# Kernel optimization log

Measured on AMD Instinct MI355X. Metric: run time of the kernel, lower is better.

## Reference

```python
import jax, jax.numpy as jnp
import numpy as np

B, S, D = 8, 1024, 1024
NEG = -1e9


def setup_inputs() -> dict:
    key = jax.random.key(0)
    ks = jax.random.split(key, 6)
    context = jax.random.normal(ks[0], (B, S, D), dtype=jnp.float32)
    eos_mask = jax.random.randint(ks[1], (B, S, S), 0, 2).astype(jnp.int32)
    scale = 1.0 / np.sqrt(D).astype(np.float32)
    Wq = jax.random.normal(ks[2], (D, D), dtype=jnp.float32) * scale
    bq = jnp.zeros((D,), jnp.float32)
    Wk = jax.random.normal(ks[3], (D, D), dtype=jnp.float32) * scale
    bk = jnp.zeros((D,), jnp.float32)
    ln_a = jnp.ones((D,), jnp.float32)
    ln_b = jnp.zeros((D,), jnp.float32)
    return dict(context=context, eos_mask=eos_mask, Wq=Wq, bq=bq, Wk=Wk, bk=bk,
                ln_a=ln_a, ln_b=ln_b)


def _forward(context, eos_mask, Wq, bq, Wk, bk, ln_a, ln_b):
    d_model = context.shape[-1]
    seq_len = context.shape[1]
    # LayerNorm with torch-style unbiased std (ddof=1)
    mean = context.mean(-1, keepdims=True)
    var = ((context - mean) ** 2).sum(-1, keepdims=True) / (d_model - 1)
    x = ln_a * (context - mean) / (jnp.sqrt(var) + 1e-6) + ln_b

    a = jnp.eye(seq_len, k=1, dtype=jnp.int32)    # super-diagonal
    b = jnp.eye(seq_len, k=0, dtype=jnp.int32)    # diagonal
    c = jnp.eye(seq_len, k=-1, dtype=jnp.int32)   # sub-diagonal
    tri = jnp.triu(jnp.ones((seq_len, seq_len), jnp.float32), 0)

    mask = eos_mask & (a + c)  # [B,S,S] banded + eos mask

    q = x @ Wq.T + bq
    k = x @ Wk.T + bk
    scores = jnp.einsum('bsd,btd->bst', q, k) / d_model
    scores = jnp.where(mask == 0, NEG, scores)
    neibor = jax.nn.softmax(scores, axis=-1)
    neibor = jnp.sqrt(neibor * jnp.swapaxes(neibor, -2, -1) + 1e-9)

    # log-space triangular matmul 'scan'
    t = jnp.where(a == 0, 0.0, jnp.log(neibor + 1e-9)) @ tri  # [B,S,S]
    g = jnp.exp(jnp.einsum('st,btu->bsu', tri, t))
    strict_upper = tri.astype(jnp.int32) - b
    g = jnp.where(strict_upper == 0, 0.0, g)
    g = g + jnp.swapaxes(g, -2, -1) + jnp.where(b == 0, 1e-9, neibor)
    return g, neibor


def reference(context, eos_mask, Wq, bq, Wk, bk, ln_a, ln_b):
    return _forward(context, eos_mask, Wq, bq, Wk, bk, ln_a, ln_b)
```

## Files before the change

### kernel.cpp

```cpp
#include <hip/hip_runtime.h>
#include <math.h>

#define B_ 8
#define S_ 1024
#define D_ 1024
constexpr int BS = B_ * S_;

typedef short bf16x8 __attribute__((ext_vector_type(8)));
typedef float f32x4 __attribute__((ext_vector_type(4)));

__device__ __forceinline__ unsigned short f2bf(float f) {
    unsigned int u = __float_as_uint(f);
    u += 0x7fffu + ((u >> 16) & 1u);
    return (unsigned short)(u >> 16);
}
__device__ __forceinline__ float bf2f(unsigned short h) {
    return __uint_as_float(((unsigned int)h) << 16);
}

__device__ __forceinline__ float block_reduce_sum(float val, float* sh) {
    int tid = threadIdx.x;
    int lane = tid & 63, w = tid >> 6;
    #pragma unroll
    for (int off = 32; off > 0; off >>= 1) val += __shfl_down(val, off, 64);
    if (lane == 0) sh[w] = val;
    __syncthreads();
    int nw = blockDim.x >> 6;
    float total = 0.f;
    for (int i = 0; i < nw; i++) total += sh[i];
    __syncthreads();
    return total;
}

__device__ __forceinline__ float wave_reduce_sum(float v) {
    #pragma unroll
    for (int off = 32; off > 0; off >>= 1) v += __shfl_xor(v, off, 64);
    return v;
}

__global__ __launch_bounds__(256) void ln_kernel(
    const float* __restrict__ ctx,
    const float* __restrict__ ln_a,
    const float* __restrict__ ln_b,
    const float* __restrict__ u,
    const float* __restrict__ v,
    unsigned short* __restrict__ xb,
    float* __restrict__ au, float* __restrict__ av) {
    int wid = threadIdx.x >> 6, lane = threadIdx.x & 63;
    int r = blockIdx.x * 4 + wid;
    const float* row = ctx + (size_t)r * D_;
    float4 x[4];
    #pragma unroll
    for (int j = 0; j < 4; j++)
        x[j] = *(const float4*)(row + lane * 4 + j * 256);
    float s = 0.f;
    #pragma unroll
    for (int j = 0; j < 4; j++) s += x[j].x + x[j].y + x[j].z + x[j].w;
    s = wave_reduce_sum(s);
    float mean = s * (1.0f / D_);
    float sq = 0.f;
    #pragma unroll
    for (int j = 0; j < 4; j++) {
        float dx = x[j].x - mean, dy = x[j].y - mean;
        float dz = x[j].z - mean, dw = x[j].w - mean;
        sq += dx * dx + dy * dy + dz * dz + dw * dw;
    }
    sq = wave_reduce_sum(sq);
    float var = sq * (1.0f / (D_ - 1));
    float inv = 1.0f / (sqrtf(var) + 1e-6f);
    float pu = 0.f, pv = 0.f;
    #pragma unroll
    for (int j = 0; j < 4; j++) {
        int d0 = lane * 4 + j * 256;
        float4 a4 = *(const float4*)(ln_a + d0);
        float4 b4 = *(const float4*)(ln_b + d0);
        float y0 = a4.x * (x[j].x - mean) * inv + b4.x;
        float y1 = a4.y * (x[j].y - mean) * inv + b4.y;
        float y2 = a4.z * (x[j].z - mean) * inv + b4.z;
        float y3 = a4.w * (x[j].w - mean) * inv + b4.w;
        ushort4 o;
        o.x = f2bf(y0); o.y = f2bf(y1); o.z = f2bf(y2); o.w = f2bf(y3);
        *(ushort4*)(xb + (size_t)r * D_ + d0) = o;
        float4 u4 = *(const float4*)(u + d0);
        float4 v4 = *(const float4*)(v + d0);
        pu += u4.x * y0 + u4.y * y1 + u4.z * y2 + u4.w * y3;
        pv += v4.x * y0 + v4.y * y1 + v4.z * y2 + v4.w * y3;
    }
    pu = wave_reduce_sum(pu);
    pv = wave_reduce_sum(pv);
    if (lane == 0) { au[r] = pu; av[r] = pv; }
}

__global__ void prep_kernel(const float* __restrict__ Wq, const float* __restrict__ Wk,
                            const float* __restrict__ bq, const float* __restrict__ bk,
                            unsigned short* __restrict__ Wqt,
                            unsigned short* __restrict__ Wkt,
                            float* __restrict__ u, float* __restrict__ v,
                            float* __restrict__ c0) {
    int bid = blockIdx.x;
    int tid = threadIdx.x;
    if (bid < 2048) {
        __shared__ float t[32][33];
        const float* in = (bid < 1024) ? Wq : Wk;
        unsigned short* out = (bid < 1024) ? Wqt : Wkt;
        int bb = bid & 1023;
        int bx = (bb & 31) * 32, by = (bb >> 5) * 32;
        int tx = tid & 31, ty = tid >> 5;
        #pragma unroll
        for (int i = 0; i < 32; i += 8)
            t[ty + i][tx] = in[(size_t)(by + ty + i) * D_ + bx + tx];
        __syncthreads();
        #pragma unroll
        for (int i = 0; i < 32; i += 8)
            out[(size_t)(bx + ty + i) * D_ + by + tx] = f2bf(t[tx][ty + i]);
    } else {
        int b = bid - 2048;
        if (b == 128) {
            __shared__ float sh2[4];
            float p = 0.f;
            #pragma unroll
            for (int i = 0; i < 4; i++) {
                int d = tid + i * 256;
                p += bq[d] * bk[d];
            }
            float tot = block_reduce_sum(p, sh2);
            if (tid == 0) atomicAdd(c0, tot);
        } else {
            float ua[4] = {}, va[4] = {};
            int d0 = b * 8;
            for (int d = d0; d < d0 + 8; d++) {
                float bqd = bq[d], bkd = bk[d];
                const float* wkr = Wk + (size_t)d * D_;
                const float* wqr = Wq + (size_t)d * D_;
                #pragma unroll
                for (int i = 0; i < 4; i++) {
                    int c = tid + i * 256;
                    ua[i] += wkr[c] * bqd;
                    va[i] += wqr[c] * bkd;
                }
            }
            #pragma unroll
            for (int i = 0; i < 4; i++) {
                atomicAdd(&u[tid + i * 256], ua[i]);
                atomicAdd(&v[tid + i * 256], va[i]);
            }
        }
    }
}

__global__ __launch_bounds__(256) void gemm_bt64(
    const unsigned short* __restrict__ A,
    const unsigned short* __restrict__ Bt,
    unsigned short* __restrict__ C,
    int M, int N, int K) {
    __shared__ __align__(16) unsigned short smem[16384];
    const int tid = threadIdx.x;
    const int wave = tid >> 6, lane = tid & 63;
    const int bm = blockIdx.y * 64, bn = blockIdx.x * 64;
    const int lrow8 = lane >> 3;
    const int pchunk = lane & 7;
    const int m_lane = lane & 15, quad = lane >> 4;
    const int wr = wave >> 1, wc = wave & 1;

    f32x4 acc[2][2] = {};

    auto stage = [&](int buf, int k0) {
        unsigned short* As = smem + buf * 8192;
        unsigned short* Bs = As + 4096;
        #pragma unroll
        for (int c = 0; c < 2; c++) {
            int row = wave * 16 + c * 8 + lrow8;
            int gchunk = pchunk ^ (row & 7);
            const unsigned short* gpA = A + (size_t)(bm + row) * K + k0 + gchunk * 8;
            const unsigned short* gpB = Bt + (size_t)(bn + row) * K + k0 + gchunk * 8;
            __builtin_amdgcn_global_load_lds(
                (const __attribute__((address_space(1))) void*)gpA,
                (__attribute__((address_space(3))) void*)(As + (wave * 16 + c * 8) * 64),
                16, 0, 0);
            __builtin_amdgcn_global_load_lds(
                (const __attribute__((address_space(1))) void*)gpB,
                (__attribute__((address_space(3))) void*)(Bs + (wave * 16 + c * 8) * 64),
                16, 0, 0);
        }
    };

    const int nt = K >> 6;
    stage(0, 0);
    __syncthreads();
    int cur = 0;
    for (int t = 0; t < nt; ++t) {
        if (t < nt - 1) stage(cur ^ 1, (t + 1) * 64);
        const unsigned short* As = smem + cur * 8192;
        const unsigned short* Bs = As + 4096;
        #pragma unroll
        for (int kk = 0; kk < 2; kk++) {
            bf16x8 af[2], bfr[2];
            #pragma unroll
            for (int i = 0; i < 2; i++) {
                int row = wr * 32 + i * 16 + m_lane;
                int lchunk = kk * 4 + quad;
                af[i] = *(const bf16x8*)(As + row * 64 + (lchunk ^ (row & 7)) * 8);
            }
            #pragma unroll
            for (int j = 0; j < 2; j++) {
                int row = wc * 32 + j * 16 + m_lane;
                int lchunk = kk * 4 + quad;
                bfr[j] = *(const bf16x8*)(Bs + row * 64 + (lchunk ^ (row & 7)) * 8);
            }
            #pragma unroll
            for (int i = 0; i < 2; i++)
                #pragma unroll
                for (int j = 0; j < 2; j++)
                    acc[i][j] = __builtin_amdgcn_mfma_f32_16x16x32_bf16(
                        af[i], bfr[j], acc[i][j], 0, 0, 0);
        }
        __syncthreads();
        cur ^= 1;
    }
    #pragma unroll
    for (int i = 0; i < 2; i++)
        #pragma unroll
        for (int j = 0; j < 2; j++)
            #pragma unroll
            for (int r = 0; r < 4; r++) {
                int row = bm + wr * 32 + i * 16 + quad * 4 + r;
                int col = bn + wc * 32 + j * 16 + m_lane;
                C[(size_t)row * N + col] = f2bf(acc[i][j][r]);
            }
}

__device__ __forceinline__ int xs_idx(int row, int col) {
    return row * 128 + (((col >> 3) ^ (row & 7)) << 3) + (col & 7);
}

__global__ __launch_bounds__(256) void gemm_fused(
    const unsigned short* __restrict__ A,
    const unsigned short* __restrict__ Bt,
    float* __restrict__ ydu, float* __restrict__ ydd,
    int M, int N, int K) {
    __shared__ __align__(16) unsigned short smem[32768];
    const int tid = threadIdx.x;
    const int wave = tid >> 6, lane = tid & 63;
    const int bid = blockIdx.x;
    const int bm = (bid & 63) * 128, bn = (bid >> 6) * 128;
    const int lrow8 = lane >> 3;
    const int pchunk = lane & 7;
    const int m_lane = lane & 15, quad = lane >> 4;
    const int wr = wave >> 1, wc = wave & 1;

    f32x4 acc[4][4] = {};

    auto stage = [&](int buf, int k0) {
        unsigned short* As = smem + buf * 16384;
        unsigned short* Bs = As + 8192;
        #pragma unroll
        for (int c = 0; c < 4; c++) {
            int row = wave * 32 + c * 8 + lrow8;
            int gchunk = pchunk ^ (row & 7);
            const unsigned short* gpA = A + (size_t)(bm + row) * K + k0 + gchunk * 8;
            __builtin_amdgcn_global_load_lds(
                (const __attribute__((address_space(1))) void*)gpA,
                (__attribute__((address_space(3))) void*)(As + (wave * 32 + c * 8) * 64),
                16, 0, 0);
            const unsigned short* gpB = Bt + (size_t)(bn + row) * K + k0 + gchunk * 8;
            __builtin_amdgcn_global_load_lds(
                (const __attribute__((address_space(1))) void*)gpB,
                (__attribute__((address_space(3))) void*)(Bs + (wave * 32 + c * 8) * 64),
                16, 0, 0);
        }
    };

    const int nt = K >> 6;
    stage(0, 0);
    __syncthreads();
    int cur = 0;
    for (int t = 0; t < nt; ++t) {
        if (t < nt - 1) stage(cur ^ 1, (t + 1) * 64);
        const unsigned short* As = smem + cur * 16384;
        const unsigned short* Bs = As + 8192;
        #pragma unroll
        for (int kk = 0; kk < 2; kk++) {
            bf16x8 af[4], bfr[4];
            #pragma unroll
            for (int i = 0; i < 4; i++) {
                int row = wr * 64 + i * 16 + m_lane;
                int lchunk = kk * 4 + quad;
                af[i] = *(const bf16x8*)(As + row * 64 + (lchunk ^ (row & 7)) * 8);
            }
            #pragma unroll
            for (int j = 0; j < 4; j++) {
                int row = wc * 64 + j * 16 + m_lane;
                int lchunk = kk * 4 + quad;
                bfr[j] = *(const bf16x8*)(Bs + row * 64 + (lchunk ^ (row & 7)) * 8);
            }
            #pragma unroll
            for (int i = 0; i < 4; i++)
                #pragma unroll
                for (int j = 0; j < 4; j++)
                    acc[i][j] = __builtin_amdgcn_mfma_f32_16x16x32_bf16(
                        af[i], bfr[j], acc[i][j], 0, 0, 0);
        }
        __syncthreads();
        cur ^= 1;
    }

    unsigned short* Xs = smem;
    #pragma unroll
    for (int it = 0; it < 8; it++) {
        int c = it * 256 + wave * 64 + lane;
        int lr = c >> 4;
        int ch = c & 15;
        int gch = ch ^ (lr & 7);
        const unsigned short* gp = A + (size_t)(bm + lr) * K + bn + gch * 8;
        __builtin_amdgcn_global_load_lds(
            (const __attribute__((address_space(1))) void*)gp,
            (__attribute__((address_space(3))) void*)(Xs + (size_t)(it * 256 + wave * 64) * 8),
            16, 0, 0);
    }
    __syncthreads();

    #pragma unroll
    for (int i = 0; i < 4; i++) {
        #pragma unroll
        for (int r = 0; r < 4; r++) {
            int lrow = wr * 64 + i * 16 + quad * 4 + r;
            int row = bm + lrow;
            int s = row & (S_ - 1);
            bool hu = (s < S_ - 1), hd = (s > 0);
            float pu = 0.f, pd = 0.f;
            #pragma unroll
            for (int j = 0; j < 4; j++) {
                int lc = wc * 64 + j * 16 + m_lane;
                float a = acc[i][j][r];
                if (hu) {
                    float xu = (lrow < 127) ? bf2f(Xs[xs_idx(lrow + 1, lc)])
                                            : bf2f(A[(size_t)(row + 1) * K + bn + lc]);
                    pu += a * xu;
                }
                if (hd) {
                    float xd = (lrow > 0) ? bf2f(Xs[xs_idx(lrow - 1, lc)])
                                          : bf2f(A[(size_t)(row - 1) * K + bn + lc]);
                    pd += a * xd;
                }
            }
            #pragma unroll
            for (int off = 1; off < 16; off <<= 1) {
                pu += __shfl_xor(pu, off, 64);
                pd += __shfl_xor(pd, off, 64);
            }
            if (m_lane == 0) {
                atomicAdd(&ydu[row], pu);
                atomicAdd(&ydd[row], pd);
            }
        }
    }
}

__global__ void softmax_prefix(const float* __restrict__ ydu, const float* __restrict__ ydd,
                               const float* __restrict__ au, const float* __restrict__ av,
                               const float* __restrict__ c0p, const int* __restrict__ eos,
                               float* __restrict__ Pup, float* __restrict__ Pdn,
                               float* __restrict__ bg, double* __restrict__ C) {
    __shared__ float pdsh[1024];
    __shared__ double wsum[16];
    int b = blockIdx.x;
    int t = threadIdx.x;
    int r = b * S_ + t;
    float c0 = *c0p;
    const float inv_d = 1.0f / D_;
    bool mu = false, md = false;
    float su = 0.f, sd = 0.f;
    if (t < S_ - 1) {
        mu = eos[(size_t)b * S_ * S_ + (size_t)t * S_ + (t + 1)] != 0;
        su = (ydu[r] + av[r] + au[r + 1] + c0) * inv_d;
    }
    if (t > 0) {
        md = eos[(size_t)b * S_ * S_ + (size_t)t * S_ + (t - 1)] != 0;
        sd = (ydd[r] + av[r] + au[r - 1] + c0) * inv_d;
    }
    float pu, pd, pb;
    if (mu && md) {
        float m = fmaxf(su, sd);
        float eu = expf(su - m), ed = expf(sd - m);
        float inv = 1.0f / (eu + ed);
        pu = eu * inv; pd = ed * inv; pb = 0.f;
    } else if (mu) { pu = 1.f; pd = 0.f; pb = 0.f; }
    else if (md)   { pu = 0.f; pd = 1.f; pb = 0.f; }
    else           { pu = pd = pb = 1.0f / S_; }
    Pup[r] = pu; Pdn[r] = pd; bg[r] = pb;
    pdsh[t] = pd;
    __syncthreads();
    double l = 0.0;
    if (t < S_ - 1) {
        float p = sqrtf(pu * pdsh[t + 1] + 1e-9f) + 1e-9f;
        l = log((double)p);
    }
    int lane = t & 63, w = t >> 6;
    double vv = l;
    #pragma unroll
    for (int off = 1; off < 64; off <<= 1) {
        double o = __shfl_up(vv, off, 64);
        if (lane >= off) vv += o;
    }
    if (lane == 63) wsum[w] = vv;
    __syncthreads();
    if (t == 0) {
        double acc = 0.0;
        #pragma unroll
        for (int i = 0; i < 16; i++) { double x = wsum[i]; wsum[i] = acc; acc += x; }
    }
    __syncthreads();
    vv += wsum[w];
    size_t base = (size_t)b * S_;
    if (t == 0) C[base] = 0.0;
    if (t < S_ - 1) C[base + t + 1] = vv;
}

__global__ void write_out(const float* __restrict__ Pup, const float* __restrict__ Pdn,
                          const float* __restrict__ bg, const double* __restrict__ C,
                          float* __restrict__ out) {
    int r = blockIdx.x;
    int b = r >> 10, s = r & (S_ - 1);
    size_t rowbase = (size_t)r * S_;
    size_t bb = (size_t)b * S_;
    float pu_s = (s < S_ - 1) ? Pup[r] : 0.f;
    float pd_s = (s > 0) ? Pdn[r] : 0.f;
    float bg_s = bg[r];
    double C_s = C[r];
    int t0 = threadIdx.x * 4;
    float* gp = out;
    float* np = out + (size_t)B_ * S_ * S_;
    float4 bgv = *(const float4*)(bg + bb + t0);
    float4 gv, nv;
    #pragma unroll
    for (int j = 0; j < 4; j++) {
        int t = t0 + j;
        float P_st = (t == s + 1) ? pu_s : ((t == s - 1) ? pd_s : bg_s);
        float P_ts;
        if (t == s - 1)      P_ts = Pup[bb + t];
        else if (t == s + 1) P_ts = Pdn[bb + t];
        else                 P_ts = ((const float*)&bgv)[j];
        float neib = sqrtf(P_st * P_ts + 1e-9f);
        float g;
        if (t == s) {
            g = neib;
        } else {
            double diff = (t > s) ? (C[bb + t] - C_s) : (C_s - C[bb + t]);
            g = expf((float)diff) + 1e-9f;
        }
        ((float*)&gv)[j] = g;
        ((float*)&nv)[j] = neib;
    }
    *(float4*)(gp + rowbase + t0) = gv;
    *(float4*)(np + rowbase + t0) = nv;
}

extern "C" void kernel_launch(void* const* d_in, const int* in_sizes, int n_in,
                              void* d_out, int out_size, void* d_ws, size_t ws_size,
                              hipStream_t stream) {
    const float* ctx  = (const float*)d_in[0];
    const int*   eos  = (const int*)d_in[1];
    const float* Wq   = (const float*)d_in[2];
    const float* bq   = (const float*)d_in[3];
    const float* Wk   = (const float*)d_in[4];
    const float* bk   = (const float*)d_in[5];
    const float* ln_a = (const float*)d_in[6];
    const float* ln_b = (const float*)d_in[7];
    float* out = (float*)d_out;

    char* ws = (char*)d_ws;
    size_t off = 0;
    auto alloc = [&](size_t bytes) {
        void* p = ws + off;
        off += (bytes + 255) & ~(size_t)255;
        return p;
    };
    unsigned short* Xb  = (unsigned short*)alloc((size_t)BS * D_ * 2);
    unsigned short* Wqt = (unsigned short*)alloc((size_t)D_ * D_ * 2);
    unsigned short* Wkt = (unsigned short*)alloc((size_t)D_ * D_ * 2);
    unsigned short* Mt  = (unsigned short*)alloc((size_t)D_ * D_ * 2);
    float*  ydu = (float*)alloc(BS * 4);
    float*  ydd = (float*)alloc(BS * 4);
    float*  u   = (float*)alloc(D_ * 4);
    float*  v   = (float*)alloc(D_ * 4);
    float*  c0  = (float*)alloc(4);
    size_t zero_bytes = (size_t)((char*)c0 - (char*)ydu) + 256;
    float*  au  = (float*)alloc(BS * 4);
    float*  av  = (float*)alloc(BS * 4);
    float*  Pup = (float*)alloc(BS * 4);
    float*  Pdn = (float*)alloc(BS * 4);
    float*  bg  = (float*)alloc(BS * 4);
    double* Cp  = (double*)alloc(BS * 8);

    hipMemsetAsync(ydu, 0, zero_bytes, stream);
    prep_kernel<<<2177, 256, 0, stream>>>(Wq, Wk, bq, bk, Wqt, Wkt, u, v, c0);
    ln_kernel<<<BS / 4, 256, 0, stream>>>(ctx, ln_a, ln_b, u, v, Xb, au, av);
    gemm_bt64<<<dim3(16, 16), 256, 0, stream>>>(Wkt, Wqt, Mt, D_, D_, D_);
    gemm_fused<<<512, 256, 0, stream>>>(Xb, Mt, ydu, ydd, BS, D_, D_);
    softmax_prefix<<<B_, 1024, 0, stream>>>(ydu, ydd, au, av, c0, eos, Pup, Pdn, bg, Cp);
    write_out<<<BS, 256, 0, stream>>>(Pup, Pdn, bg, Cp, out);
}
```

Measured before the change: 197.1 us.

## Merge LayerNorm with weight GEMM launch and replace atomics with partial buffers

```diff
diff --git a/kernel.cpp b/kernel.cpp
--- a/kernel.cpp
+++ b/kernel.cpp
@@ -36,59 +36,6 @@
     #pragma unroll
     for (int off = 32; off > 0; off >>= 1) v += __shfl_xor(v, off, 64);
     return v;
-}
-
-__global__ __launch_bounds__(256) void ln_kernel(
-    const float* __restrict__ ctx,
-    const float* __restrict__ ln_a,
-    const float* __restrict__ ln_b,
-    const float* __restrict__ u,
-    const float* __restrict__ v,
-    unsigned short* __restrict__ xb,
-    float* __restrict__ au, float* __restrict__ av) {
-    int wid = threadIdx.x >> 6, lane = threadIdx.x & 63;
-    int r = blockIdx.x * 4 + wid;
-    const float* row = ctx + (size_t)r * D_;
-    float4 x[4];
-    #pragma unroll
-    for (int j = 0; j < 4; j++)
-        x[j] = *(const float4*)(row + lane * 4 + j * 256);
-    float s = 0.f;
-    #pragma unroll
-    for (int j = 0; j < 4; j++) s += x[j].x + x[j].y + x[j].z + x[j].w;
-    s = wave_reduce_sum(s);
-    float mean = s * (1.0f / D_);
-    float sq = 0.f;
-    #pragma unroll
-    for (int j = 0; j < 4; j++) {
-        float dx = x[j].x - mean, dy = x[j].y - mean;
-        float dz = x[j].z - mean, dw = x[j].w - mean;
-        sq += dx * dx + dy * dy + dz * dz + dw * dw;
-    }
-    sq = wave_reduce_sum(sq);
-    float var = sq * (1.0f / (D_ - 1));
-    float inv = 1.0f / (sqrtf(var) + 1e-6f);
-    float pu = 0.f, pv = 0.f;
-    #pragma unroll
-    for (int j = 0; j < 4; j++) {
-        int d0 = lane * 4 + j * 256;
-        float4 a4 = *(const float4*)(ln_a + d0);
-        float4 b4 = *(const float4*)(ln_b + d0);
-        float y0 = a4.x * (x[j].x - mean) * inv + b4.x;
-        float y1 = a4.y * (x[j].y - mean) * inv + b4.y;
-        float y2 = a4.z * (x[j].z - mean) * inv + b4.z;
-        float y3 = a4.w * (x[j].w - mean) * inv + b4.w;
-        ushort4 o;
-        o.x = f2bf(y0); o.y = f2bf(y1); o.z = f2bf(y2); o.w = f2bf(y3);
-        *(ushort4*)(xb + (size_t)r * D_ + d0) = o;
-        float4 u4 = *(const float4*)(u + d0);
-        float4 v4 = *(const float4*)(v + d0);
-        pu += u4.x * y0 + u4.y * y1 + u4.z * y2 + u4.w * y3;
-        pv += v4.x * y0 + v4.y * y1 + v4.z * y2 + v4.w * y3;
-    }
-    pu = wave_reduce_sum(pu);
-    pv = wave_reduce_sum(pv);
-    if (lane == 0) { au[r] = pu; av[r] = pv; }
 }
 
 __global__ void prep_kernel(const float* __restrict__ Wq, const float* __restrict__ Wk,
@@ -113,120 +60,168 @@
         #pragma unroll
         for (int i = 0; i < 32; i += 8)
             out[(size_t)(bx + ty + i) * D_ + by + tx] = f2bf(t[tx][ty + i]);
+    } else if (bid < 2112) {
+        __shared__ float shu[16][17], shv[16][17];
+        int g = bid - 2048;
+        int cbase = g * 16;
+        int cc = tid & 15, dg = tid >> 4;
+        float ua = 0.f, va = 0.f;
+        for (int d = dg; d < D_; d += 16) {
+            ua += Wk[(size_t)d * D_ + cbase + cc] * bq[d];
+            va += Wq[(size_t)d * D_ + cbase + cc] * bk[d];
+        }
+        shu[dg][cc] = ua; shv[dg][cc] = va;
+        __syncthreads();
+        if (tid < 16) {
+            float su_ = 0.f, sv_ = 0.f;
+            #pragma unroll
+            for (int k = 0; k < 16; k++) { su_ += shu[k][tid]; sv_ += shv[k][tid]; }
+            u[cbase + tid] = su_;
+            v[cbase + tid] = sv_;
+        }
     } else {
-        int b = bid - 2048;
-        if (b == 128) {
-            __shared__ float sh2[4];
-            float p = 0.f;
-            #pragma unroll
-            for (int i = 0; i < 4; i++) {
-                int d = tid + i * 256;
-                p += bq[d] * bk[d];
-            }
-            float tot = block_reduce_sum(p, sh2);
-            if (tid == 0) atomicAdd(c0, tot);
-        } else {
-            float ua[4] = {}, va[4] = {};
-            int d0 = b * 8;
-            for (int d = d0; d < d0 + 8; d++) {
-                float bqd = bq[d], bkd = bk[d];
-                const float* wkr = Wk + (size_t)d * D_;
-                const float* wqr = Wq + (size_t)d * D_;
-                #pragma unroll
-                for (int i = 0; i < 4; i++) {
-                    int c = tid + i * 256;
-                    ua[i] += wkr[c] * bqd;
-                    va[i] += wqr[c] * bkd;
-                }
-            }
-            #pragma unroll
-            for (int i = 0; i < 4; i++) {
-                atomicAdd(&u[tid + i * 256], ua[i]);
-                atomicAdd(&v[tid + i * 256], va[i]);
-            }
-        }
-    }
-}
-
-__global__ __launch_bounds__(256) void gemm_bt64(
+        __shared__ float sh2[4];
+        float p = 0.f;
+        #pragma unroll
+        for (int i = 0; i < 4; i++) {
+            int d = tid + i * 256;
+            p += bq[d] * bk[d];
+        }
+        float tot = block_reduce_sum(p, sh2);
+        if (tid == 0) c0[0] = tot;
+    }
+}
+
+__global__ __launch_bounds__(256) void ln_bt64(
+    const float* __restrict__ ctx,
+    const float* __restrict__ ln_a, const float* __restrict__ ln_b,
+    const float* __restrict__ u, const float* __restrict__ v,
+    unsigned short* __restrict__ xb,
+    float* __restrict__ au, float* __restrict__ av,
     const unsigned short* __restrict__ A,
     const unsigned short* __restrict__ Bt,
-    unsigned short* __restrict__ C,
-    int M, int N, int K) {
+    unsigned short* __restrict__ C) {
     __shared__ __align__(16) unsigned short smem[16384];
+    const int bid = blockIdx.x;
     const int tid = threadIdx.x;
-    const int wave = tid >> 6, lane = tid & 63;
-    const int bm = blockIdx.y * 64, bn = blockIdx.x * 64;
-    const int lrow8 = lane >> 3;
-    const int pchunk = lane & 7;
-    const int m_lane = lane & 15, quad = lane >> 4;
-    const int wr = wave >> 1, wc = wave & 1;
-
-    f32x4 acc[2][2] = {};
-
-    auto stage = [&](int buf, int k0) {
-        unsigned short* As = smem + buf * 8192;
-        unsigned short* Bs = As + 4096;
-        #pragma unroll
-        for (int c = 0; c < 2; c++) {
-            int row = wave * 16 + c * 8 + lrow8;
-            int gchunk = pchunk ^ (row & 7);
-            const unsigned short* gpA = A + (size_t)(bm + row) * K + k0 + gchunk * 8;
-            const unsigned short* gpB = Bt + (size_t)(bn + row) * K + k0 + gchunk * 8;
-            __builtin_amdgcn_global_load_lds(
-                (const __attribute__((address_space(1))) void*)gpA,
-                (__attribute__((address_space(3))) void*)(As + (wave * 16 + c * 8) * 64),
-                16, 0, 0);
-            __builtin_amdgcn_global_load_lds(
-                (const __attribute__((address_space(1))) void*)gpB,
-                (__attribute__((address_space(3))) void*)(Bs + (wave * 16 + c * 8) * 64),
-                16, 0, 0);
-        }
-    };
-
-    const int nt = K >> 6;
-    stage(0, 0);
-    __syncthreads();
-    int cur = 0;
-    for (int t = 0; t < nt; ++t) {
-        if (t < nt - 1) stage(cur ^ 1, (t + 1) * 64);
-        const unsigned short* As = smem + cur * 8192;
-        const unsigned short* Bs = As + 4096;
-        #pragma unroll
-        for (int kk = 0; kk < 2; kk++) {
-            bf16x8 af[2], bfr[2];
-            #pragma unroll
-            for (int i = 0; i < 2; i++) {
-                int row = wr * 32 + i * 16 + m_lane;
-                int lchunk = kk * 4 + quad;
-                af[i] = *(const bf16x8*)(As + row * 64 + (lchunk ^ (row & 7)) * 8);
-            }
-            #pragma unroll
-            for (int j = 0; j < 2; j++) {
-                int row = wc * 32 + j * 16 + m_lane;
-                int lchunk = kk * 4 + quad;
-                bfr[j] = *(const bf16x8*)(Bs + row * 64 + (lchunk ^ (row & 7)) * 8);
-            }
-            #pragma unroll
-            for (int i = 0; i < 2; i++)
+    if (bid < 256) {
+        const int wave = tid >> 6, lane = tid & 63;
+        const int bm = (bid >> 4) * 64, bn = (bid & 15) * 64;
+        const int lrow8 = lane >> 3;
+        const int pchunk = lane & 7;
+        const int m_lane = lane & 15, quad = lane >> 4;
+        const int wr = wave >> 1, wc = wave & 1;
+
+        f32x4 acc[2][2] = {};
+
+        auto stage = [&](int buf, int k0) {
+            unsigned short* As = smem + buf * 8192;
+            unsigned short* Bs = As + 4096;
+            #pragma unroll
+            for (int c = 0; c < 2; c++) {
+                int row = wave * 16 + c * 8 + lrow8;
+                int gchunk = pchunk ^ (row & 7);
+                const unsigned short* gpA = A + (size_t)(bm + row) * D_ + k0 + gchunk * 8;
+                const unsigned short* gpB = Bt + (size_t)(bn + row) * D_ + k0 + gchunk * 8;
+                __builtin_amdgcn_global_load_lds(
+                    (const __attribute__((address_space(1))) void*)gpA,
+                    (__attribute__((address_space(3))) void*)(As + (wave * 16 + c * 8) * 64),
+                    16, 0, 0);
+                __builtin_amdgcn_global_load_lds(
+                    (const __attribute__((address_space(1))) void*)gpB,
+                    (__attribute__((address_space(3))) void*)(Bs + (wave * 16 + c * 8) * 64),
+                    16, 0, 0);
+            }
+        };
+
+        const int nt = D_ >> 6;
+        stage(0, 0);
+        __syncthreads();
+        int cur = 0;
+        for (int t = 0; t < nt; ++t) {
+            if (t < nt - 1) stage(cur ^ 1, (t + 1) * 64);
+            const unsigned short* As = smem + cur * 8192;
+            const unsigned short* Bs = As + 4096;
+            #pragma unroll
+            for (int kk = 0; kk < 2; kk++) {
+                bf16x8 af[2], bfr[2];
                 #pragma unroll
-                for (int j = 0; j < 2; j++)
-                    acc[i][j] = __builtin_amdgcn_mfma_f32_16x16x32_bf16(
-                        af[i], bfr[j], acc[i][j], 0, 0, 0);
-        }
-        __syncthreads();
-        cur ^= 1;
-    }
-    #pragma unroll
-    for (int i = 0; i < 2; i++)
-        #pragma unroll
-        for (int j = 0; j < 2; j++)
-            #pragma unroll
-            for (int r = 0; r < 4; r++) {
-                int row = bm + wr * 32 + i * 16 + quad * 4 + r;
-                int col = bn + wc * 32 + j * 16 + m_lane;
-                C[(size_t)row * N + col] = f2bf(acc[i][j][r]);
-            }
+                for (int i = 0; i < 2; i++) {
+                    int row = wr * 32 + i * 16 + m_lane;
+                    int lchunk = kk * 4 + quad;
+                    af[i] = *(const bf16x8*)(As + row * 64 + (lchunk ^ (row & 7)) * 8);
+                }
+                #pragma unroll
+                for (int j = 0; j < 2; j++) {
+                    int row = wc * 32 + j * 16 + m_lane;
+                    int lchunk = kk * 4 + quad;
+                    bfr[j] = *(const bf16x8*)(Bs + row * 64 + (lchunk ^ (row & 7)) * 8);
+                }
+                #pragma unroll
+                for (int i = 0; i < 2; i++)
+                    #pragma unroll
+                    for (int j = 0; j < 2; j++)
+                        acc[i][j] = __builtin_amdgcn_mfma_f32_16x16x32_bf16(
+                            af[i], bfr[j], acc[i][j], 0, 0, 0);
+            }
+            __syncthreads();
+            cur ^= 1;
+        }
+        #pragma unroll
+        for (int i = 0; i < 2; i++)
+            #pragma unroll
+            for (int j = 0; j < 2; j++)
+                #pragma unroll
+                for (int r = 0; r < 4; r++) {
+                    int row = bm + wr * 32 + i * 16 + quad * 4 + r;
+                    int col = bn + wc * 32 + j * 16 + m_lane;
+                    C[(size_t)row * D_ + col] = f2bf(acc[i][j][r]);
+                }
+    } else {
+        int wid = tid >> 6, lane = tid & 63;
+        int r = (bid - 256) * 4 + wid;
+        const float* row = ctx + (size_t)r * D_;
+        float4 x[4];
+        #pragma unroll
+        for (int j = 0; j < 4; j++)
+            x[j] = *(const float4*)(row + lane * 4 + j * 256);
+        float s = 0.f;
+        #pragma unroll
+        for (int j = 0; j < 4; j++) s += x[j].x + x[j].y + x[j].z + x[j].w;
+        s = wave_reduce_sum(s);
+        float mean = s * (1.0f / D_);
+        float sq = 0.f;
+        #pragma unroll
+        for (int j = 0; j < 4; j++) {
+            float dx = x[j].x - mean, dy = x[j].y - mean;
+            float dz = x[j].z - mean, dw = x[j].w - mean;
+            sq += dx * dx + dy * dy + dz * dz + dw * dw;
+        }
+        sq = wave_reduce_sum(sq);
+        float var = sq * (1.0f / (D_ - 1));
+        float inv = 1.0f / (sqrtf(var) + 1e-6f);
+        float pu = 0.f, pv = 0.f;
+        #pragma unroll
+        for (int j = 0; j < 4; j++) {
+            int d0 = lane * 4 + j * 256;
+            float4 a4 = *(const float4*)(ln_a + d0);
+            float4 b4 = *(const float4*)(ln_b + d0);
+            float y0 = a4.x * (x[j].x - mean) * inv + b4.x;
+            float y1 = a4.y * (x[j].y - mean) * inv + b4.y;
+            float y2 = a4.z * (x[j].z - mean) * inv + b4.z;
+            float y3 = a4.w * (x[j].w - mean) * inv + b4.w;
+            ushort4 o;
+            o.x = f2bf(y0); o.y = f2bf(y1); o.z = f2bf(y2); o.w = f2bf(y3);
+            *(ushort4*)(xb + (size_t)r * D_ + d0) = o;
+            float4 u4 = *(const float4*)(u + d0);
+            float4 v4 = *(const float4*)(v + d0);
+            pu += u4.x * y0 + u4.y * y1 + u4.z * y2 + u4.w * y3;
+            pv += v4.x * y0 + v4.y * y1 + v4.z * y2 + v4.w * y3;
+        }
+        pu = wave_reduce_sum(pu);
+        pv = wave_reduce_sum(pv);
+        if (lane == 0) { au[r] = pu; av[r] = pv; }
+    }
 }
 
 __device__ __forceinline__ int xs_idx(int row, int col) {
@@ -236,7 +231,7 @@
 __global__ __launch_bounds__(256) void gemm_fused(
     const unsigned short* __restrict__ A,
     const unsigned short* __restrict__ Bt,
-    float* __restrict__ ydu, float* __restrict__ ydd,
+    float* __restrict__ ydu_part, float* __restrict__ ydd_part,
     int M, int N, int K) {
     __shared__ __align__(16) unsigned short smem[32768];
     const int tid = threadIdx.x;
@@ -319,6 +314,7 @@
     }
     __syncthreads();
 
+    const int part = (bid >> 6) * 2 + wc;
     #pragma unroll
     for (int i = 0; i < 4; i++) {
         #pragma unroll
@@ -349,14 +345,15 @@
                 pd += __shfl_xor(pd, off, 64);
             }
             if (m_lane == 0) {
-                atomicAdd(&ydu[row], pu);
-                atomicAdd(&ydd[row], pd);
-            }
-        }
-    }
-}
-
-__global__ void softmax_prefix(const float* __restrict__ ydu, const float* __restrict__ ydd,
+                ydu_part[(size_t)part * BS + row] = pu;
+                ydd_part[(size_t)part * BS + row] = pd;
+            }
+        }
+    }
+}
+
+__global__ void softmax_prefix(const float* __restrict__ ydu_part,
+                               const float* __restrict__ ydd_part,
                                const float* __restrict__ au, const float* __restrict__ av,
                                const float* __restrict__ c0p, const int* __restrict__ eos,
                                float* __restrict__ Pup, float* __restrict__ Pdn,
@@ -372,11 +369,17 @@
     float su = 0.f, sd = 0.f;
     if (t < S_ - 1) {
         mu = eos[(size_t)b * S_ * S_ + (size_t)t * S_ + (t + 1)] != 0;
-        su = (ydu[r] + av[r] + au[r + 1] + c0) * inv_d;
+        float s_ = 0.f;
+        #pragma unroll
+        for (int j = 0; j < 16; j++) s_ += ydu_part[(size_t)j * BS + r];
+        su = (s_ + av[r] + au[r + 1] + c0) * inv_d;
     }
     if (t > 0) {
         md = eos[(size_t)b * S_ * S_ + (size_t)t * S_ + (t - 1)] != 0;
-        sd = (ydd[r] + av[r] + au[r - 1] + c0) * inv_d;
+        float s_ = 0.f;
+        #pragma unroll
+        for (int j = 0; j < 16; j++) s_ += ydd_part[(size_t)j * BS + r];
+        sd = (s_ + av[r] + au[r - 1] + c0) * inv_d;
     }
     float pu, pd, pb;
     if (mu && md) {
@@ -479,12 +482,11 @@
     unsigned short* Wqt = (unsigned short*)alloc((size_t)D_ * D_ * 2);
     unsigned short* Wkt = (unsigned short*)alloc((size_t)D_ * D_ * 2);
     unsigned short* Mt  = (unsigned short*)alloc((size_t)D_ * D_ * 2);
-    float*  ydu = (float*)alloc(BS * 4);
-    float*  ydd = (float*)alloc(BS * 4);
+    float*  ydu_part = (float*)alloc((size_t)16 * BS * 4);
+    float*  ydd_part = (float*)alloc((size_t)16 * BS * 4);
     float*  u   = (float*)alloc(D_ * 4);
     float*  v   = (float*)alloc(D_ * 4);
     float*  c0  = (float*)alloc(4);
-    size_t zero_bytes = (size_t)((char*)c0 - (char*)ydu) + 256;
     float*  au  = (float*)alloc(BS * 4);
     float*  av  = (float*)alloc(BS * 4);
     float*  Pup = (float*)alloc(BS * 4);
@@ -492,11 +494,11 @@
     float*  bg  = (float*)alloc(BS * 4);
     double* Cp  = (double*)alloc(BS * 8);
 
-    hipMemsetAsync(ydu, 0, zero_bytes, stream);
-    prep_kernel<<<2177, 256, 0, stream>>>(Wq, Wk, bq, bk, Wqt, Wkt, u, v, c0);
-    ln_kernel<<<BS / 4, 256, 0, stream>>>(ctx, ln_a, ln_b, u, v, Xb, au, av);
-    gemm_bt64<<<dim3(16, 16), 256, 0, stream>>>(Wkt, Wqt, Mt, D_, D_, D_);
-    gemm_fused<<<512, 256, 0, stream>>>(Xb, Mt, ydu, ydd, BS, D_, D_);
-    softmax_prefix<<<B_, 1024, 0, stream>>>(ydu, ydd, au, av, c0, eos, Pup, Pdn, bg, Cp);
+    prep_kernel<<<2113, 256, 0, stream>>>(Wq, Wk, bq, bk, Wqt, Wkt, u, v, c0);
+    ln_bt64<<<2304, 256, 0, stream>>>(ctx, ln_a, ln_b, u, v, Xb, au, av,
+                                      Wkt, Wqt, Mt);
+    gemm_fused<<<512, 256, 0, stream>>>(Xb, Mt, ydu_part, ydd_part, BS, D_, D_);
+    softmax_prefix<<<B_, 1024, 0, stream>>>(ydu_part, ydd_part, au, av, c0, eos,
+                                            Pup, Pdn, bg, Cp);
     write_out<<<BS, 256, 0, stream>>>(Pup, Pdn, bg, Cp, out);
 }
```

After: 202.0 us. 2.5% more time.
